# Kernel tuning notes

Hardware: AMD Instinct MI355X
Metric: run time of the kernel (lower is better)

The kernel has to match this reference:

```python
import jax, jax.numpy as jnp
import numpy as np

N_NODES = 10000
N_EDGES = 160000
R_CUT = 1.4415
N_RBF = 20


def silu(x):
    return x * jax.nn.sigmoid(x)


def setup_inputs() -> dict:
    key = jax.random.key(0)
    ks = jax.random.split(key, 12)
    x = jax.random.normal(ks[0], (N_NODES, 512), jnp.float32)
    edge_index = jax.random.randint(ks[1], (2, N_EDGES), 0, N_NODES, dtype=jnp.int64)
    ea1 = jax.random.normal(ks[2], (N_EDGES, 3), jnp.float32)
    edge_attr1 = ea1 / jnp.linalg.norm(ea1, axis=1, keepdims=True)  # unit edge vectors
    # edge lengths in (0.1, 1.4) so bessel 1/r is well-conditioned and inside r_cut
    edge_attr2 = jax.random.uniform(ks[3], (N_EDGES,), jnp.float32) * 1.3 + 0.1

    def lin(k, fi, fo):
        return (jax.random.normal(k, (fi, fo), jnp.float32) / np.sqrt(fi)).astype(jnp.float32)

    return {
        "x": x, "edge_index": edge_index,
        "edge_attr1": edge_attr1, "edge_attr2": edge_attr2,
        # PAINNMessage params (stored [in,out]; y = x @ W + b)
        "W1": lin(ks[4], 128, 128), "b1": jnp.zeros(128, jnp.float32),
        "W2": lin(ks[5], 20, 384), "b2": jnp.zeros(384, jnp.float32),
        "W3": lin(ks[6], 128, 384), "b3": jnp.zeros(384, jnp.float32),
        # PAINNUpdate params
        "U": lin(ks[7], 128, 128), "V": lin(ks[8], 128, 128),
        "Wu1": lin(ks[9], 256, 128), "bu1": jnp.zeros(128, jnp.float32),
        "Wu2": lin(ks[10], 128, 384), "bu2": jnp.zeros(384, jnp.float32),
    }


def _painn_block(x, edge_index, edge_attr1, edge_attr2,
                 W1, b1, W2, b2, W3, b3, U, V, Wu1, bu1, Wu2, bu2):
    src, dst = edge_index[0], edge_index[1]
    E = src.shape[0]

    # ---------- PAINNMessage ----------
    x_j = x[src]                                   # gather [E,512]
    v_j = x_j[:, :384].reshape(E, 128, 3)          # vector channels
    s_j = x_j[:, 384:]                             # scalar channels [E,128]
    s_j = silu(s_j @ W1 + b1) @ W3 + b3            # [E,384]

    r = edge_attr2[:, None]                        # [E,1]
    n = jnp.arange(1, N_RBF + 1, dtype=x.dtype)    # [20]
    rbf = jnp.sqrt(2.0 / R_CUT) * jnp.sin(n * jnp.pi * r / R_CUT) / r  # [E,20]
    cutoff = 0.5 * (jnp.cos(jnp.pi * r / R_CUT) + 1.0) * (r < R_CUT)
    edge_basis = (rbf * cutoff) @ W2 + b2          # [E,384]

    split = s_j * edge_basis
    s1, s2, s3 = split[:, :128], split[:, 128:256], split[:, 256:]
    # v_j * split_1 + outer(split_3, unit_edge_vec)
    v_msg = v_j * s1[:, :, None] + s3[:, :, None] * edge_attr1[:, None, :]  # [E,128,3]
    msg = jnp.concatenate([v_msg.reshape(E, 384), s2], axis=1)              # [E,512]
    x = x + jax.ops.segment_sum(msg, dst, num_segments=N_NODES)

    # ---------- PAINNUpdate ----------
    x_j = x[src]                                   # [E,512]
    v = x_j[:, :384].reshape(E, 3, 128)            # (torch .view semantics)
    v = v @ U                                      # [E,3,128]
    v_V = v @ V                                    # [E,3,128]
    v = v.reshape(E, 128, 3)                       # plain reshape, as in torch .view
    v_V = v_V.reshape(E, 128, 3)
    norm = jnp.linalg.norm(v_V, axis=2)            # [E,128]
    s = x_j[:, 384:]
    h = silu(jnp.concatenate([norm, s], axis=1) @ Wu1 + bu1) @ Wu2 + bu2  # [E,384]
    s1, s2, s3 = h[:, :128], h[:, 128:256], h[:, 256:]  # s2 is unused in original
    v = v * s1[:, :, None]
    dot = jnp.einsum('ijk,ijk->ij', v, v_V)        # [E,128]
    scal = dot + s3                                # [E,128]
    msg = jnp.concatenate([v.reshape(E, 384), scal], axis=1)  # [E,512]
    x = x + jax.ops.segment_sum(msg, dst, num_segments=N_NODES)
    return x


def reference(x, edge_index, edge_attr1, edge_attr2,
              W1, b1, W2, b2, W3, b3, U, V, Wu1, bu1, Wu2, bu2):
    return _painn_block(x, edge_index, edge_attr1, edge_attr2,
                        W1, b1, W2, b2, W3, b3, U, V, Wu1, bu1, Wu2, bu2)
```

## Files before the change

### kernel.cpp

```cpp
#include <hip/hip_runtime.h>
#include <hip/hip_bf16.h>

#define N_NODES 10000
#define N_EDGES 160000
#define FEAT 512
#define D 128
#define NRBF 20
#define RCUT 1.4415f
#define CAP 64

typedef __attribute__((ext_vector_type(8))) short bf16x8;
typedef __attribute__((ext_vector_type(4))) float f32x4;

__device__ __forceinline__ float silu_f(float x) { return x / (1.0f + __expf(-x)); }
__device__ __forceinline__ float s2f(short s) {
    unsigned int u = ((unsigned int)(unsigned short)s) << 16;
    float f; __builtin_memcpy(&f, &u, 4); return f;
}
__device__ __forceinline__ short f2s(float f) {
    __hip_bfloat16 h = __float2bfloat16(f);
    short s; __builtin_memcpy(&s, &h, 2); return s;
}

__global__ __launch_bounds__(256) void k_zero_ints(int* __restrict__ p, int n) {
    int i = blockIdx.x * blockDim.x + threadIdx.x;
    if (i < n) p[i] = 0;
}

__global__ __launch_bounds__(256) void k_fill(const int* __restrict__ ei,
                                              int* __restrict__ cnt,
                                              unsigned int* __restrict__ slot) {
    int e = blockIdx.x * blockDim.x + threadIdx.x;
    if (e < N_EDGES) {
        int d = ei[N_EDGES + e];
        int pos = atomicAdd(&cnt[d], 1);
        if (pos < CAP)
            slot[d * CAP + pos] = (((unsigned int)e) << 14) | (unsigned int)ei[e];
    }
}

__global__ __launch_bounds__(256) void k_basis(const float* __restrict__ ea2,
                                               __hip_bfloat16* __restrict__ basis) {
    int i = blockIdx.x * blockDim.x + threadIdx.x;
    if (i < N_EDGES * NRBF) {
        int e = i / NRBF, n = i % NRBF;
        float r  = ea2[e];
        float pr = 3.14159265358979f * r / RCUT;
        float rbf = sqrtf(2.0f / RCUT) * __sinf((float)(n + 1) * pr) / r;
        float cut = 0.5f * (__cosf(pr) + 1.0f) * (r < RCUT ? 1.0f : 0.0f);
        basis[i] = __float2bfloat16(rbf * cut);
    }
}

__global__ __launch_bounds__(256) void k_pack(const float* __restrict__ W,
                                              short* __restrict__ Wp,
                                              int K, int N) {
    int idx = blockIdx.x * 256 + threadIdx.x;
    int NT = N >> 4;
    int total = (K >> 5) * NT * 64;
    if (idx >= total) return;
    int lane = idx & 63;
    int fid  = idx >> 6;
    int ks = fid / NT, ct = fid % NT;
    int k0 = ks * 32 + ((lane >> 4) << 3);
    int c  = ct * 16 + (lane & 15);
    short* o = Wp + (size_t)idx * 8;
    #pragma unroll
    for (int j = 0; j < 8; ++j)
        o[j] = f2s(W[(size_t)(k0 + j) * N + c]);
}

#define LDSP 136
__global__ __launch_bounds__(256) void k_A_mfma(
    const float* __restrict__ x,
    const short* __restrict__ W1p, const float* __restrict__ b1,
    const short* __restrict__ W3p, const float* __restrict__ b3,
    __hip_bfloat16* __restrict__ P1)
{
    __shared__ __align__(16) short sj[16 * LDSP];
    __shared__ __align__(16) short tt[16 * LDSP];
    const int t = threadIdx.x;
    const int lane = t & 63, wave = t >> 6;
    const int n0 = blockIdx.x * 16;

    for (int i = t; i < 16 * 128; i += 256) {
        int e = i >> 7, j = i & 127;
        sj[e * LDSP + j] = f2s(x[(size_t)(n0 + e) * FEAT + 384 + j]);
    }
    for (int i = t; i < 16 * 384; i += 256) {
        int e = i / 384, o = i % 384;
        int j = o & 127, c = o >> 7;
        P1[(size_t)(n0 + e) * 768 + 384 + o] =
            __float2bfloat16(x[(size_t)(n0 + e) * FEAT + 3 * j + c]);
    }
    __syncthreads();

    {
        f32x4 acc[2];
        #pragma unroll
        for (int q = 0; q < 2; ++q) acc[q] = (f32x4){0.f, 0.f, 0.f, 0.f};
        for (int ks = 0; ks < 4; ++ks) {
            bf16x8 a = *(const bf16x8*)&sj[(lane & 15) * LDSP + ks * 32 + ((lane >> 4) << 3)];
            #pragma unroll
            for (int q = 0; q < 2; ++q) {
                bf16x8 b = ((const bf16x8*)W1p)[((size_t)ks * 8 + wave * 2 + q) * 64 + lane];
                acc[q] = __builtin_amdgcn_mfma_f32_16x16x32_bf16(a, b, acc[q], 0, 0, 0);
            }
        }
        #pragma unroll
        for (int q = 0; q < 2; ++q) {
            int col = (wave * 2 + q) * 16 + (lane & 15);
            int row = (lane >> 4) << 2;
            float bb = b1[col];
            #pragma unroll
            for (int r = 0; r < 4; ++r)
                tt[(row + r) * LDSP + col] = f2s(silu_f(acc[q][r] + bb));
        }
    }
    __syncthreads();

    {
        f32x4 acc[6];
        #pragma unroll
        for (int q = 0; q < 6; ++q) acc[q] = (f32x4){0.f, 0.f, 0.f, 0.f};
        for (int ks = 0; ks < 4; ++ks) {
            bf16x8 a = *(const bf16x8*)&tt[(lane & 15) * LDSP + ks * 32 + ((lane >> 4) << 3)];
            #pragma unroll
            for (int q = 0; q < 6; ++q) {
                bf16x8 b = ((const bf16x8*)W3p)[((size_t)ks * 24 + wave * 6 + q) * 64 + lane];
                acc[q] = __builtin_amdgcn_mfma_f32_16x16x32_bf16(a, b, acc[q], 0, 0, 0);
            }
        }
        #pragma unroll
        for (int q = 0; q < 6; ++q) {
            int col = (wave * 6 + q) * 16 + (lane & 15);
            int row = (lane >> 4) << 2;
            float bb = b3[col];
            #pragma unroll
            for (int r = 0; r < 4; ++r)
                P1[(size_t)(n0 + row + r) * 768 + col] = __float2bfloat16(acc[q][r] + bb);
        }
    }
}

__global__ __launch_bounds__(256) void k_B_mfma(
    const short* __restrict__ Up, const short* __restrict__ Vp,
    const short* __restrict__ Wu1p, const float* __restrict__ bu1,
    const short* __restrict__ Wu2p, const float* __restrict__ bu2,
    const float* __restrict__ xin,
    __hip_bfloat16* __restrict__ M2)
{
    __shared__ __align__(16) short XV[48 * LDSP];
    __shared__ __align__(16) short VU[48 * LDSP];
    __shared__ __align__(16) short S [16 * LDSP];
    __shared__ __align__(16) short NRM[16 * LDSP];
    __shared__ __align__(16) short H1[16 * LDSP];
    __shared__ __align__(16) short A1[16 * LDSP];
    __shared__ __align__(16) short A3[16 * LDSP];

    const int t = threadIdx.x, lane = t & 63, wave = t >> 6;
    const int n0 = blockIdx.x * 16;

    for (int i = t; i < 16 * 512; i += 256) {
        int e = i >> 9, f = i & 511;
        short sv = f2s(xin[(size_t)(n0 + e) * FEAT + f]);
        if (f < 384) XV[(e * 3 + (f >> 7)) * LDSP + (f & 127)] = sv;
        else         S[e * LDSP + (f - 384)] = sv;
    }
    __syncthreads();

    {
        f32x4 acc[3][2];
        #pragma unroll
        for (int rt = 0; rt < 3; ++rt)
            #pragma unroll
            for (int q = 0; q < 2; ++q) acc[rt][q] = (f32x4){0.f, 0.f, 0.f, 0.f};
        for (int ks = 0; ks < 4; ++ks) {
            bf16x8 b[2];
            #pragma unroll
            for (int q = 0; q < 2; ++q)
                b[q] = ((const bf16x8*)Up)[((size_t)ks * 8 + wave * 2 + q) * 64 + lane];
            #pragma unroll
            for (int rt = 0; rt < 3; ++rt) {
                bf16x8 a = *(const bf16x8*)&XV[(rt * 16 + (lane & 15)) * LDSP + ks * 32 + ((lane >> 4) << 3)];
                #pragma unroll
                for (int q = 0; q < 2; ++q)
                    acc[rt][q] = __builtin_amdgcn_mfma_f32_16x16x32_bf16(a, b[q], acc[rt][q], 0, 0, 0);
            }
        }
        #pragma unroll
        for (int rt = 0; rt < 3; ++rt)
            #pragma unroll
            for (int q = 0; q < 2; ++q) {
                int col = (wave * 2 + q) * 16 + (lane & 15);
                int row = rt * 16 + ((lane >> 4) << 2);
                #pragma unroll
                for (int r = 0; r < 4; ++r)
                    VU[(row + r) * LDSP + col] = f2s(acc[rt][q][r]);
            }
    }
    __syncthreads();

    {
        f32x4 acc[3][2];
        #pragma unroll
        for (int rt = 0; rt < 3; ++rt)
            #pragma unroll
            for (int q = 0; q < 2; ++q) acc[rt][q] = (f32x4){0.f, 0.f, 0.f, 0.f};
        for (int ks = 0; ks < 4; ++ks) {
            bf16x8 b[2];
            #pragma unroll
            for (int q = 0; q < 2; ++q)
                b[q] = ((const bf16x8*)Vp)[((size_t)ks * 8 + wave * 2 + q) * 64 + lane];
            #pragma unroll
            for (int rt = 0; rt < 3; ++rt) {
                bf16x8 a = *(const bf16x8*)&VU[(rt * 16 + (lane & 15)) * LDSP + ks * 32 + ((lane >> 4) << 3)];
                #pragma unroll
                for (int q = 0; q < 2; ++q)
                    acc[rt][q] = __builtin_amdgcn_mfma_f32_16x16x32_bf16(a, b[q], acc[rt][q], 0, 0, 0);
            }
        }
        __syncthreads();
        #pragma unroll
        for (int rt = 0; rt < 3; ++rt)
            #pragma unroll
            for (int q = 0; q < 2; ++q) {
                int col = (wave * 2 + q) * 16 + (lane & 15);
                int row = rt * 16 + ((lane >> 4) << 2);
                #pragma unroll
                for (int r = 0; r < 4; ++r)
                    XV[(row + r) * LDSP + col] = f2s(acc[rt][q][r]);
            }
    }
    __syncthreads();

    for (int i = t; i < 16 * 128; i += 256) {
        int nl = i >> 7, j = i & 127;
        float s = 0.f;
        #pragma unroll
        for (int c = 0; c < 3; ++c) {
            int q = 3 * j + c;
            float f = s2f(XV[(nl * 3 + (q >> 7)) * LDSP + (q & 127)]);
            s += f * f;
        }
        NRM[nl * LDSP + j] = f2s(sqrtf(s));
    }
    __syncthreads();

    {
        f32x4 acc[2];
        #pragma unroll
        for (int q = 0; q < 2; ++q) acc[q] = (f32x4){0.f, 0.f, 0.f, 0.f};
        for (int ks = 0; ks < 8; ++ks) {
            const short* asrc = (ks < 4) ? NRM : S;
            int k0 = (ks & 3) * 32;
            bf16x8 a = *(const bf16x8*)&asrc[(lane & 15) * LDSP + k0 + ((lane >> 4) << 3)];
            #pragma unroll
            for (int q = 0; q < 2; ++q) {
                bf16x8 b = ((const bf16x8*)Wu1p)[((size_t)ks * 8 + wave * 2 + q) * 64 + lane];
                acc[q] = __builtin_amdgcn_mfma_f32_16x16x32_bf16(a, b, acc[q], 0, 0, 0);
            }
        }
        #pragma unroll
        for (int q = 0; q < 2; ++q) {
            int col = (wave * 2 + q) * 16 + (lane & 15);
            int row = (lane >> 4) << 2;
            float bb = bu1[col];
            #pragma unroll
            for (int r = 0; r < 4; ++r)
                H1[(row + r) * LDSP + col] = f2s(silu_f(acc[q][r] + bb));
        }
    }
    __syncthreads();

    {
        f32x4 acc[4];
        #pragma unroll
        for (int q = 0; q < 4; ++q) acc[q] = (f32x4){0.f, 0.f, 0.f, 0.f};
        for (int ks = 0; ks < 4; ++ks) {
            bf16x8 a = *(const bf16x8*)&H1[(lane & 15) * LDSP + ks * 32 + ((lane >> 4) << 3)];
            #pragma unroll
            for (int q = 0; q < 4; ++q) {
                int w = wave * 4 + q;
                int ctp = (w < 8) ? w : (16 + (w - 8));
                bf16x8 b = ((const bf16x8*)Wu2p)[((size_t)ks * 24 + ctp) * 64 + lane];
                acc[q] = __builtin_amdgcn_mfma_f32_16x16x32_bf16(a, b, acc[q], 0, 0, 0);
            }
        }
        #pragma unroll
        for (int q = 0; q < 4; ++q) {
            int w = wave * 4 + q;
            int colloc = (w & 7) * 16 + (lane & 15);
            int row = (lane >> 4) << 2;
            short* dst = (w < 8) ? A1 : A3;
            float bb = bu2[((w < 8) ? 0 : 256) + colloc];
            #pragma unroll
            for (int r = 0; r < 4; ++r)
                dst[(row + r) * LDSP + colloc] = f2s(acc[q][r] + bb);
        }
    }
    __syncthreads();

    for (int i = t; i < 16 * 128; i += 256) {
        int nl = i >> 7, j = i & 127;
        float a1v = s2f(A1[nl * LDSP + j]);
        float a3v = s2f(A3[nl * LDSP + j]);
        __hip_bfloat16* mrow = M2 + (size_t)(n0 + nl) * FEAT;
        float dot = 0.f;
        #pragma unroll
        for (int c = 0; c < 3; ++c) {
            int q = 3 * j + c;
            int rr = nl * 3 + (q >> 7), cc = q & 127;
            float vu_ = s2f(VU[rr * LDSP + cc]);
            float vv_ = s2f(XV[rr * LDSP + cc]);
            float vf = vu_ * a1v;
            dot += vf * vv_;
            mrow[c * 128 + j] = __float2bfloat16(vf);
        }
        mrow[384 + j] = __float2bfloat16(dot + a3v);
    }
}

__global__ __launch_bounds__(128) void k_gather1(
    const float* __restrict__ x,
    const __hip_bfloat16* __restrict__ P1,
    const __hip_bfloat16* __restrict__ basis,
    const float* __restrict__ ea1,
    const float* __restrict__ W2, const float* __restrict__ b2,
    const int* __restrict__ cnt, const unsigned int* __restrict__ slot,
    float* __restrict__ out)
{
    __shared__ float ebl[CAP][NRBF];
    __shared__ float eall[CAP][3];
    __shared__ int srcl[CAP], ell[CAP];

    const int d = blockIdx.x, t = threadIdx.x;

    float w2r0[NRBF], w2r1[NRBF], w2r2[NRBF];
    #pragma unroll
    for (int n = 0; n < NRBF; ++n) {
        w2r0[n] = W2[n * 384 + t];
        w2r1[n] = W2[n * 384 + 128 + t];
        w2r2[n] = W2[n * 384 + 256 + t];
    }
    const float b2a = b2[t], b2b = b2[128 + t], b2c = b2[256 + t];

    const int deg = min(cnt[d], CAP);
    if (t < deg) {
        unsigned int p = slot[d * CAP + t];
        srcl[t] = (int)(p & 16383u);
        ell[t]  = (int)(p >> 14);
    }
    __syncthreads();
    for (int i = t; i < deg * NRBF; i += 128)
        ebl[i / NRBF][i % NRBF] = __bfloat162float(basis[(size_t)ell[i / NRBF] * NRBF + (i % NRBF)]);
    for (int i = t; i < deg * 3; i += 128)
        eall[i / 3][i % 3] = ea1[(size_t)ell[i / 3] * 3 + (i % 3)];
    __syncthreads();

    float acc0 = 0.f, acc1 = 0.f, acc2 = 0.f, accs = 0.f;

    for (int base = 0; base < deg; base += 8) {
        float fr[8][6];
        #pragma unroll
        for (int ee = 0; ee < 8; ++ee) {
            int idx = (base + ee < deg) ? (base + ee) : base;
            const __hip_bfloat16* R = P1 + (size_t)srcl[idx] * 768;
            fr[ee][0] = __bfloat162float(R[t]);
            fr[ee][1] = __bfloat162float(R[128 + t]);
            fr[ee][2] = __bfloat162float(R[256 + t]);
            fr[ee][3] = __bfloat162float(R[384 + t]);
            fr[ee][4] = __bfloat162float(R[512 + t]);
            fr[ee][5] = __bfloat162float(R[640 + t]);
        }
        #pragma unroll
        for (int ee = 0; ee < 8; ++ee) {
            if (base + ee >= deg) break;
            const int ix = base + ee;
            float ebA = b2a, ebB = b2b, ebC = b2c;
            #pragma unroll
            for (int n = 0; n < NRBF; ++n) {
                float e = ebl[ix][n];
                ebA += e * w2r0[n];
                ebB += e * w2r1[n];
                ebC += e * w2r2[n];
            }
            float s1 = fr[ee][0] * ebA;
            float s2 = fr[ee][1] * ebB;
            float s3 = fr[ee][2] * ebC;
            acc0 += fr[ee][3] * s1 + s3 * eall[ix][0];
            acc1 += fr[ee][4] * s1 + s3 * eall[ix][1];
            acc2 += fr[ee][5] * s1 + s3 * eall[ix][2];
            accs += s2;
        }
    }

    const size_t ro = (size_t)d * FEAT;
    out[ro + 3 * t]     = x[ro + 3 * t]     + acc0;
    out[ro + 3 * t + 1] = x[ro + 3 * t + 1] + acc1;
    out[ro + 3 * t + 2] = x[ro + 3 * t + 2] + acc2;
    out[ro + 384 + t]   = x[ro + 384 + t]   + accs;
}

__global__ __launch_bounds__(256) void k_gather2(
    const __hip_bfloat16* __restrict__ M2,
    const int* __restrict__ cnt, const unsigned int* __restrict__ slot,
    float* __restrict__ out)
{
    __shared__ float row[FEAT];
    __shared__ int sl[CAP];
    const int d = blockIdx.x, t = threadIdx.x;
    const int deg = min(cnt[d], CAP);
    if (t < deg) sl[t] = (int)(slot[d * CAP + t] & 16383u);
    __syncthreads();

    float a0 = 0.0f, a1 = 0.0f;
    int i = 0;
    for (; i + 8 <= deg; i += 8) {
        __hip_bfloat162 v[8];
        #pragma unroll
        for (int q = 0; q < 8; ++q)
            v[q] = ((const __hip_bfloat162*)(M2 + (size_t)sl[i + q] * FEAT))[t];
        #pragma unroll
        for (int q = 0; q < 8; ++q) {
            a0 += __bfloat162float(v[q].x);
            a1 += __bfloat162float(v[q].y);
        }
    }
    for (; i < deg; ++i) {
        __hip_bfloat162 v = ((const __hip_bfloat162*)(M2 + (size_t)sl[i] * FEAT))[t];
        a0 += __bfloat162float(v.x);
        a1 += __bfloat162float(v.y);
    }
    row[2 * t]     = a0;
    row[2 * t + 1] = a1;
    __syncthreads();
    #pragma unroll
    for (int gi = 0; gi < 2; ++gi) {
        int g = t + gi * 256;
        int m = (g < 384) ? ((g % 3) * 128 + g / 3) : g;
        out[(size_t)d * FEAT + g] += row[m];
    }
}

extern "C" void kernel_launch(void* const* d_in, const int* in_sizes, int n_in,
                              void* d_out, int out_size, void* d_ws, size_t ws_size,
                              hipStream_t stream) {
    (void)in_sizes; (void)n_in; (void)out_size; (void)ws_size;
    const float* x   = (const float*)d_in[0];
    const int*   ei  = (const int*)d_in[1];
    const float* ea1 = (const float*)d_in[2];
    const float* ea2 = (const float*)d_in[3];
    const float* W1  = (const float*)d_in[4];
    const float* b1  = (const float*)d_in[5];
    const float* W2  = (const float*)d_in[6];
    const float* b2  = (const float*)d_in[7];
    const float* W3  = (const float*)d_in[8];
    const float* b3  = (const float*)d_in[9];
    const float* U   = (const float*)d_in[10];
    const float* V   = (const float*)d_in[11];
    const float* Wu1 = (const float*)d_in[12];
    const float* bu1 = (const float*)d_in[13];
    const float* Wu2 = (const float*)d_in[14];
    const float* bu2 = (const float*)d_in[15];
    float* out = (float*)d_out;

    char* w = (char*)d_ws;
    __hip_bfloat16* P1    = (__hip_bfloat16*)w;
    __hip_bfloat16* M2    = (__hip_bfloat16*)(w + 15360000);
    __hip_bfloat16* basis = (__hip_bfloat16*)(w + 25600000);
    short* W1p  = (short*)(w + 32000000);
    short* W3p  = (short*)(w + 32032768);
    short* Upk  = (short*)(w + 32131072);
    short* Vpk  = (short*)(w + 32163840);
    short* Wu1p = (short*)(w + 32196608);
    short* Wu2p = (short*)(w + 32262144);
    int*          cnt  = (int*)(w + 32360448);
    unsigned int* slot = (unsigned int*)(w + 32400448);

    k_pack<<<8,  256, 0, stream>>>(W1,  W1p,  128, 128);
    k_pack<<<24, 256, 0, stream>>>(W3,  W3p,  128, 384);
    k_pack<<<8,  256, 0, stream>>>(U,   Upk,  128, 128);
    k_pack<<<8,  256, 0, stream>>>(V,   Vpk,  128, 128);
    k_pack<<<16, 256, 0, stream>>>(Wu1, Wu1p, 256, 128);
    k_pack<<<24, 256, 0, stream>>>(Wu2, Wu2p, 128, 384);

    k_zero_ints<<<(N_NODES + 255) / 256,        256, 0, stream>>>(cnt, N_NODES);
    k_fill     <<<(N_EDGES + 255) / 256,        256, 0, stream>>>(ei, cnt, slot);
    k_basis    <<<(N_EDGES * NRBF + 255) / 256, 256, 0, stream>>>(ea2, basis);

    k_A_mfma   <<<N_NODES / 16, 256, 0, stream>>>(x, W1p, b1, W3p, b3, P1);
    k_gather1  <<<N_NODES,      128, 0, stream>>>(x, P1, basis, ea1, W2, b2, cnt, slot, out);
    k_B_mfma   <<<N_NODES / 16, 256, 0, stream>>>(Upk, Vpk, Wu1p, bu1, Wu2p, bu2, out, M2);
    k_gather2  <<<N_NODES,      256, 0, stream>>>(M2, cnt, slot, out);
}
```

Baseline: 256.1 us.

## Use MFMA for edge-basis projection and interleave P1 layout for vector gather loads

Merges the six weight-pack launches into one, fuses edge-slot filling with basis computation (sin values built by Chebyshev recurrence), and replaces the memset kernel with hipMemsetAsync. In the gather kernel, the per-edge 20x384 basis projection moves from scalar FMAs with W2 held in registers to a bf16 MFMA over 16-edge chunks staged through LDS. P1 is re-laid out so each thread pulls its six bf16 values with a single 16-byte load. The trade-offs are more LDS, extra barriers per chunk, and bf16 rounding of W2.

```diff
diff --git a/kernel.cpp b/kernel.cpp
--- a/kernel.cpp
+++ b/kernel.cpp
@@ -21,53 +21,69 @@
     __hip_bfloat16 h = __float2bfloat16(f);
     short s; __builtin_memcpy(&s, &h, 2); return s;
 }
-
-__global__ __launch_bounds__(256) void k_zero_ints(int* __restrict__ p, int n) {
-    int i = blockIdx.x * blockDim.x + threadIdx.x;
-    if (i < n) p[i] = 0;
-}
-
-__global__ __launch_bounds__(256) void k_fill(const int* __restrict__ ei,
-                                              int* __restrict__ cnt,
-                                              unsigned int* __restrict__ slot) {
-    int e = blockIdx.x * blockDim.x + threadIdx.x;
-    if (e < N_EDGES) {
-        int d = ei[N_EDGES + e];
-        int pos = atomicAdd(&cnt[d], 1);
-        if (pos < CAP)
-            slot[d * CAP + pos] = (((unsigned int)e) << 14) | (unsigned int)ei[e];
-    }
-}
-
-__global__ __launch_bounds__(256) void k_basis(const float* __restrict__ ea2,
-                                               __hip_bfloat16* __restrict__ basis) {
-    int i = blockIdx.x * blockDim.x + threadIdx.x;
-    if (i < N_EDGES * NRBF) {
-        int e = i / NRBF, n = i % NRBF;
-        float r  = ea2[e];
-        float pr = 3.14159265358979f * r / RCUT;
-        float rbf = sqrtf(2.0f / RCUT) * __sinf((float)(n + 1) * pr) / r;
-        float cut = 0.5f * (__cosf(pr) + 1.0f) * (r < RCUT ? 1.0f : 0.0f);
-        basis[i] = __float2bfloat16(rbf * cut);
-    }
-}
-
-__global__ __launch_bounds__(256) void k_pack(const float* __restrict__ W,
-                                              short* __restrict__ Wp,
-                                              int K, int N) {
-    int idx = blockIdx.x * 256 + threadIdx.x;
+__device__ __forceinline__ float asf(unsigned int u) {
+    float f; __builtin_memcpy(&f, &u, 4); return f;
+}
+
+__global__ __launch_bounds__(256) void k_fill_basis(
+    const int* __restrict__ ei, const float* __restrict__ ea2,
+    int* __restrict__ cnt, unsigned int* __restrict__ slot,
+    __hip_bfloat16* __restrict__ basis)
+{
+    int e = blockIdx.x * 256 + threadIdx.x;
+    if (e >= N_EDGES) return;
+    int d = ei[N_EDGES + e];
+    int pos = atomicAdd(&cnt[d], 1);
+    if (pos < CAP)
+        slot[d * CAP + pos] = (((unsigned int)e) << 14) | (unsigned int)ei[e];
+
+    float r  = ea2[e];
+    float pr = 3.14159265358979f * r / RCUT;
+    float cosv = __cosf(pr);
+    float cut  = 0.5f * (cosv + 1.0f) * (r < RCUT ? 1.0f : 0.0f);
+    float pref = sqrtf(2.0f / RCUT) / r * cut;
+    float c2 = 2.0f * cosv;
+    float sm1 = 0.0f, s = __sinf(pr);
+    #pragma unroll
+    for (int n = 0; n < NRBF; ++n) {
+        basis[(size_t)e * NRBF + n] = __float2bfloat16(pref * s);
+        float nx = c2 * s - sm1; sm1 = s; s = nx;
+    }
+}
+
+__global__ __launch_bounds__(256) void k_pack_all(
+    const float* __restrict__ W1, const float* __restrict__ W3,
+    const float* __restrict__ U,  const float* __restrict__ V,
+    const float* __restrict__ Wu1, const float* __restrict__ Wu2,
+    const float* __restrict__ W2,
+    short* __restrict__ W1p, short* __restrict__ W3p,
+    short* __restrict__ Up,  short* __restrict__ Vp,
+    short* __restrict__ Wu1p, short* __restrict__ Wu2p,
+    short* __restrict__ W2p)
+{
+    int b = blockIdx.x;
+    const float* W; short* Wp; int K, N, Kreal;
+    if      (b < 8)  { W = W1;  Wp = W1p;  K = 128; N = 128; Kreal = 128; }
+    else if (b < 32) { W = W3;  Wp = W3p;  K = 128; N = 384; Kreal = 128; b -= 8;  }
+    else if (b < 40) { W = U;   Wp = Up;   K = 128; N = 128; Kreal = 128; b -= 32; }
+    else if (b < 48) { W = V;   Wp = Vp;   K = 128; N = 128; Kreal = 128; b -= 40; }
+    else if (b < 64) { W = Wu1; Wp = Wu1p; K = 256; N = 128; Kreal = 256; b -= 48; }
+    else if (b < 88) { W = Wu2; Wp = Wu2p; K = 128; N = 384; Kreal = 128; b -= 64; }
+    else             { W = W2;  Wp = W2p;  K = 32;  N = 384; Kreal = 20;  b -= 88; }
+    int idx = b * 256 + threadIdx.x;
     int NT = N >> 4;
     int total = (K >> 5) * NT * 64;
     if (idx >= total) return;
-    int lane = idx & 63;
-    int fid  = idx >> 6;
+    int lane = idx & 63, fid = idx >> 6;
     int ks = fid / NT, ct = fid % NT;
     int k0 = ks * 32 + ((lane >> 4) << 3);
     int c  = ct * 16 + (lane & 15);
     short* o = Wp + (size_t)idx * 8;
     #pragma unroll
-    for (int j = 0; j < 8; ++j)
-        o[j] = f2s(W[(size_t)(k0 + j) * N + c]);
+    for (int j = 0; j < 8; ++j) {
+        int k = k0 + j;
+        o[j] = (k < Kreal) ? f2s(W[(size_t)k * N + c]) : (short)0;
+    }
 }
 
 #define LDSP 136
@@ -90,7 +106,7 @@
     for (int i = t; i < 16 * 384; i += 256) {
         int e = i / 384, o = i % 384;
         int j = o & 127, c = o >> 7;
-        P1[(size_t)(n0 + e) * 768 + 384 + o] =
+        P1[(size_t)(n0 + e) * 1024 + j * 8 + 3 + c] =
             __float2bfloat16(x[(size_t)(n0 + e) * FEAT + 3 * j + c]);
     }
     __syncthreads();
@@ -138,7 +154,8 @@
             float bb = b3[col];
             #pragma unroll
             for (int r = 0; r < 4; ++r)
-                P1[(size_t)(n0 + row + r) * 768 + col] = __float2bfloat16(acc[q][r] + bb);
+                P1[(size_t)(n0 + row + r) * 1024 + (col & 127) * 8 + (col >> 7)] =
+                    __float2bfloat16(acc[q][r] + bb);
         }
     }
 }
@@ -321,76 +338,84 @@
     }
 }
 
+#define EBST 394
 __global__ __launch_bounds__(128) void k_gather1(
     const float* __restrict__ x,
     const __hip_bfloat16* __restrict__ P1,
     const __hip_bfloat16* __restrict__ basis,
     const float* __restrict__ ea1,
-    const float* __restrict__ W2, const float* __restrict__ b2,
+    const short* __restrict__ W2p, const float* __restrict__ b2,
     const int* __restrict__ cnt, const unsigned int* __restrict__ slot,
     float* __restrict__ out)
 {
-    __shared__ float ebl[CAP][NRBF];
+    __shared__ __align__(16) short basA[CAP * 32];
+    __shared__ __align__(16) float ebL[16 * EBST];
     __shared__ float eall[CAP][3];
     __shared__ int srcl[CAP], ell[CAP];
 
     const int d = blockIdx.x, t = threadIdx.x;
-
-    float w2r0[NRBF], w2r1[NRBF], w2r2[NRBF];
+    const int lane = t & 63, wave = t >> 6;
+    const int deg = min(cnt[d], CAP);
+
     #pragma unroll
-    for (int n = 0; n < NRBF; ++n) {
-        w2r0[n] = W2[n * 384 + t];
-        w2r1[n] = W2[n * 384 + 128 + t];
-        w2r2[n] = W2[n * 384 + 256 + t];
-    }
-    const float b2a = b2[t], b2b = b2[128 + t], b2c = b2[256 + t];
-
-    const int deg = min(cnt[d], CAP);
+    for (int i = t; i < CAP * 32; i += 128) basA[i] = 0;
     if (t < deg) {
         unsigned int p = slot[d * CAP + t];
         srcl[t] = (int)(p & 16383u);
         ell[t]  = (int)(p >> 14);
     }
     __syncthreads();
-    for (int i = t; i < deg * NRBF; i += 128)
-        ebl[i / NRBF][i % NRBF] = __bfloat162float(basis[(size_t)ell[i / NRBF] * NRBF + (i % NRBF)]);
+    for (int i = t; i < deg * 32; i += 128) {
+        int e = i >> 5, k = i & 31;
+        if (k < NRBF)
+            basA[i] = ((const short*)basis)[(size_t)ell[e] * NRBF + k];
+    }
     for (int i = t; i < deg * 3; i += 128)
         eall[i / 3][i % 3] = ea1[(size_t)ell[i / 3] * 3 + (i % 3)];
     __syncthreads();
 
     float acc0 = 0.f, acc1 = 0.f, acc2 = 0.f, accs = 0.f;
 
-    for (int base = 0; base < deg; base += 8) {
-        float fr[8][6];
-        #pragma unroll
-        for (int ee = 0; ee < 8; ++ee) {
-            int idx = (base + ee < deg) ? (base + ee) : base;
-            const __hip_bfloat16* R = P1 + (size_t)srcl[idx] * 768;
-            fr[ee][0] = __bfloat162float(R[t]);
-            fr[ee][1] = __bfloat162float(R[128 + t]);
-            fr[ee][2] = __bfloat162float(R[256 + t]);
-            fr[ee][3] = __bfloat162float(R[384 + t]);
-            fr[ee][4] = __bfloat162float(R[512 + t]);
-            fr[ee][5] = __bfloat162float(R[640 + t]);
-        }
-        #pragma unroll
-        for (int ee = 0; ee < 8; ++ee) {
-            if (base + ee >= deg) break;
+    for (int base = 0; base < deg; base += 16) {
+        uint4 fr[16];
+        #pragma unroll
+        for (int ee = 0; ee < 16; ++ee) {
+            int idx = base + ee; if (idx >= deg) idx = base;
+            fr[ee] = *(const uint4*)(P1 + (size_t)srcl[idx] * 1024 + t * 8);
+        }
+        if (base) __syncthreads();
+
+        {
+            bf16x8 a = *(const bf16x8*)&basA[(base + (lane & 15)) * 32 + ((lane >> 4) << 3)];
+            #pragma unroll
+            for (int q = 0; q < 12; ++q) {
+                int tile = wave * 12 + q;
+                bf16x8 b = ((const bf16x8*)W2p)[tile * 64 + lane];
+                f32x4 acc = (f32x4){0.f, 0.f, 0.f, 0.f};
+                acc = __builtin_amdgcn_mfma_f32_16x16x32_bf16(a, b, acc, 0, 0, 0);
+                int col = tile * 16 + (lane & 15);
+                int row = (lane >> 4) << 2;
+                float bb = b2[col];
+                #pragma unroll
+                for (int r = 0; r < 4; ++r)
+                    ebL[(row + r) * EBST + col] = acc[r] + bb;
+            }
+        }
+        __syncthreads();
+
+        const int nch = min(16, deg - base);
+        for (int ee = 0; ee < nch; ++ee) {
+            uint4 u = fr[ee];
+            float a1 = asf(u.x << 16), a2 = asf(u.x & 0xffff0000u);
+            float a3 = asf(u.y << 16), x0 = asf(u.y & 0xffff0000u);
+            float x1 = asf(u.z << 16), x2 = asf(u.z & 0xffff0000u);
+            float s1 = a1 * ebL[ee * EBST + t];
+            float s2 = a2 * ebL[ee * EBST + 128 + t];
+            float s3 = a3 * ebL[ee * EBST + 256 + t];
             const int ix = base + ee;
-            float ebA = b2a, ebB = b2b, ebC = b2c;
-            #pragma unroll
-            for (int n = 0; n < NRBF; ++n) {
-                float e = ebl[ix][n];
-                ebA += e * w2r0[n];
-                ebB += e * w2r1[n];
-                ebC += e * w2r2[n];
-            }
-            float s1 = fr[ee][0] * ebA;
-            float s2 = fr[ee][1] * ebB;
-            float s3 = fr[ee][2] * ebC;
-            acc0 += fr[ee][3] * s1 + s3 * eall[ix][0];
-            acc1 += fr[ee][4] * s1 + s3 * eall[ix][1];
-            acc2 += fr[ee][5] * s1 + s3 * eall[ix][2];
+            acc0 += x0 * s1 + s3 * eall[ix][0];
+            acc1 += x1 * s1 + s3 * eall[ix][1];
+            acc2 += x2 * s1 + s3 * eall[ix][2];
             accs += s2;
         }
     }
@@ -467,30 +492,25 @@
 
     char* w = (char*)d_ws;
     __hip_bfloat16* P1    = (__hip_bfloat16*)w;
-    __hip_bfloat16* M2    = (__hip_bfloat16*)(w + 15360000);
-    __hip_bfloat16* basis = (__hip_bfloat16*)(w + 25600000);
-    short* W1p  = (short*)(w + 32000000);
-    short* W3p  = (short*)(w + 32032768);
-    short* Upk  = (short*)(w + 32131072);
-    short* Vpk  = (short*)(w + 32163840);
-    short* Wu1p = (short*)(w + 32196608);
-    short* Wu2p = (short*)(w + 32262144);
-    int*          cnt  = (int*)(w + 32360448);
-    unsigned int* slot = (unsigned int*)(w + 32400448);
-
-    k_pack<<<8,  256, 0, stream>>>(W1,  W1p,  128, 128);
-    k_pack<<<24, 256, 0, stream>>>(W3,  W3p,  128, 384);
-    k_pack<<<8,  256, 0, stream>>>(U,   Upk,  128, 128);
-    k_pack<<<8,  256, 0, stream>>>(V,   Vpk,  128, 128);
-    k_pack<<<16, 256, 0, stream>>>(Wu1, Wu1p, 256, 128);
-    k_pack<<<24, 256, 0, stream>>>(Wu2, Wu2p, 128, 384);
-
-    k_zero_ints<<<(N_NODES + 255) / 256,        256, 0, stream>>>(cnt, N_NODES);
-    k_fill     <<<(N_EDGES + 255) / 256,        256, 0, stream>>>(ei, cnt, slot);
-    k_basis    <<<(N_EDGES * NRBF + 255) / 256, 256, 0, stream>>>(ea2, basis);
-
-    k_A_mfma   <<<N_NODES / 16, 256, 0, stream>>>(x, W1p, b1, W3p, b3, P1);
-    k_gather1  <<<N_NODES,      128, 0, stream>>>(x, P1, basis, ea1, W2, b2, cnt, slot, out);
-    k_B_mfma   <<<N_NODES / 16, 256, 0, stream>>>(Upk, Vpk, Wu1p, bu1, Wu2p, bu2, out, M2);
-    k_gather2  <<<N_NODES,      256, 0, stream>>>(M2, cnt, slot, out);
-}
+    __hip_bfloat16* M2    = (__hip_bfloat16*)(w + 20480000);
+    __hip_bfloat16* basis = (__hip_bfloat16*)(w + 30720000);
+    short* W1p  = (short*)(w + 37120000);
+    short* W3p  = (short*)(w + 37152768);
+    short* Upk  = (short*)(w + 37251072);
+    short* Vpk  = (short*)(w + 37283840);
+    short* Wu1p = (short*)(w + 37316608);
+    short* Wu2p = (short*)(w + 37382144);
+    short* W2p  = (short*)(w + 37480448);
+    int*          cnt  = (int*)(w + 37505024);
+    unsigned int* slot = (unsigned int*)(w + 37545024);
+
+    hipMemsetAsync(cnt, 0, N_NODES * sizeof(int), stream);
+    k_pack_all  <<<94,  256, 0, stream>>>(W1, W3, U, V, Wu1, Wu2, W2,
+                                          W1p, W3p, Upk, Vpk, Wu1p, Wu2p, W2p);
+    k_fill_basis<<<(N_EDGES + 255) / 256, 256, 0, stream>>>(ei, ea2, cnt, slot, basis);
+
+    k_A_mfma    <<<N_NODES / 16, 256, 0, stream>>>(x, W1p, b1, W3p, b3, P1);
+    k_gather1   <<<N_NODES,      128, 0, stream>>>(x, P1, basis, ea1, W2p, b2, cnt, slot, out);
+    k_B_mfma    <<<N_NODES / 16, 256, 0, stream>>>(Upk, Vpk, Wu1p, bu1, Wu2p, bu2, out, M2);
+    k_gather2   <<<N_NODES,      256, 0, stream>>>(M2, cnt, slot, out);
+}
```

Result: slower. 361.4 us (+41.1%).
